# Kernel tuning notes

Hardware: AMD Instinct MI355X
Metric: run time of the kernel (lower is better)

Reference implementation:

```python
import jax, jax.numpy as jnp
import numpy as np

D = 1024   # feature_dim
K = 10     # num_anchors
B = 16384  # batch
H = 8      # num_heads


def setup_inputs() -> dict:
    key = jax.random.key(0)
    ks = jax.random.split(key, 12)
    f32 = jnp.float32

    def w(k, shape, scale=0.02):
        return (jax.random.normal(k, shape, f32) * scale)

    return {
        "features": jax.random.normal(ks[0], (B, D), f32),
        "anchors": w(ks[1], (K, D), 0.1),
        # anchor_refiner: Linear(D, D//2) -> ReLU -> Linear(D//2, D) -> Tanh
        "ar_w1": w(ks[2], (D, D // 2)), "ar_b1": jnp.zeros((D // 2,), f32),
        "ar_w2": w(ks[3], (D // 2, D)), "ar_b2": jnp.zeros((D,), f32),
        # attention projections
        "q_w": w(ks[4], (D, D)), "q_b": jnp.zeros((D,), f32),
        "k_w": w(ks[5], (D, D)), "k_b": jnp.zeros((D,), f32),
        "v_w": w(ks[6], (D, D)), "v_b": jnp.zeros((D,), f32),
        "o_w": w(ks[7], (D, D)), "o_b": jnp.zeros((D,), f32),
        # feature_enhancer: LayerNorm -> Linear(D,2D) -> GELU -> Linear(2D,D)
        "ln_g": jnp.ones((D,), f32), "ln_b": jnp.zeros((D,), f32),
        "ff_w1": w(ks[8], (D, 2 * D)), "ff_b1": jnp.zeros((2 * D,), f32),
        "ff_w2": w(ks[9], (2 * D, D)), "ff_b2": jnp.zeros((D,), f32),
        "div_w": jnp.asarray(0.001, f32),
        "cen_w": jnp.asarray(0.001, f32),
    }


def _l2norm(x, eps=1e-8):
    n = jnp.linalg.norm(x, axis=-1, keepdims=True)
    return x / jnp.maximum(n, eps)


def _layernorm(x, g, b, eps=1e-5):
    mu = jnp.mean(x, axis=-1, keepdims=True)
    var = jnp.mean(jnp.square(x - mu), axis=-1, keepdims=True)
    return (x - mu) * jax.lax.rsqrt(var + eps) * g + b


def reference(features, anchors, ar_w1, ar_b1, ar_w2, ar_b2,
              q_w, q_b, k_w, k_b, v_w, v_b, o_w, o_b,
              ln_g, ln_b, ff_w1, ff_b1, ff_w2, ff_b2, div_w, cen_w):
    b = features.shape[0]
    hd = D // H
    fn = _l2norm(features)                                 # [B, D]

    # anchor refinement
    refin = jnp.tanh(jax.nn.relu(anchors @ ar_w1 + ar_b1) @ ar_w2 + ar_b2)
    an = _l2norm(anchors + 0.1 * refin)                    # [K, D]

    # multi-head cross-attention to anchors
    q = (fn @ q_w + q_b).reshape(b, H, hd)                 # [B, H, hd]
    k = (an @ k_w + k_b).reshape(K, H, hd)                 # [K, H, hd]
    v = (an @ v_w + v_b).reshape(K, H, hd)
    scores = jnp.einsum('bhd,khd->bhk', q, k) / jnp.sqrt(jnp.asarray(hd, fn.dtype))
    aw = jax.nn.softmax(scores, axis=-1)                   # [B, H, K]
    att = jnp.einsum('bhk,khd->bhd', aw, v).reshape(b, D)
    att = att @ o_w + o_b

    # feature enhancer (dropout inactive: eval mode)
    enh = fn + 0.1 * att
    h = jax.nn.gelu(_layernorm(enh, ln_g, ln_b) @ ff_w1 + ff_b1, approximate=False)
    enh = h @ ff_w2 + ff_b2
    final = fn + 0.2 * enh                                 # [B, D]

    # diversity loss: pdist over K=10 anchors (45 pairs)
    diff = an[:, None, :] - an[None, :, :]                 # [K, K, D]
    dmat = jnp.sqrt(jnp.maximum(jnp.sum(diff * diff, -1), 1e-24))
    iu = np.triu_indices(K, 1)
    div_loss = jnp.exp(-jnp.maximum(dmat[iu].mean(), 1e-6))

    # center loss: attention-weighted feature-anchor distances
    avg_att = aw.mean(axis=1)                              # [B, K]
    sq = (jnp.sum(fn * fn, 1, keepdims=True) + jnp.sum(an * an, 1)
          - 2.0 * fn @ an.T)
    fa_dist = jnp.sqrt(jnp.maximum(sq, 1e-12))             # [B, K]
    center_loss = jnp.sum(avg_att * fa_dist, axis=1).mean()

    geo = jnp.abs(div_w) * div_loss + jnp.abs(cen_w) * center_loss
    geo = jnp.clip(geo, 0.0, 0.01)
    return final, geo
```

## Files before the change

### kernel.cpp

```cpp
#include <hip/hip_runtime.h>
#include <hip/hip_bf16.h>
#include <math.h>

typedef __hip_bfloat16 bf16;

#define D_  1024
#define K_  10
#define B_  16384
#define H_  8
#define HD_ 128

struct alignas(16) BF8 { bf16 v[8]; };
struct alignas(8)  BF4 { bf16 v[4]; };

typedef __bf16 bf8v __attribute__((ext_vector_type(8)));
typedef float  f4v  __attribute__((ext_vector_type(4)));

__device__ __forceinline__ float b2f(bf16 x){ return __bfloat162float(x); }
__device__ __forceinline__ bf16  f2b(float x){ return __float2bfloat16(x); }

#define GL2LDS16(g, l) __builtin_amdgcn_global_load_lds( \
    (__attribute__((address_space(1))) void*)(g), \
    (__attribute__((address_space(3))) void*)(l), 16, 0, 0)

__global__ __launch_bounds__(256) void l2norm_k(const float* __restrict__ x,
                                                bf16* __restrict__ fnb) {
  int b = blockIdx.x, t = threadIdx.x;
  float4 v = ((const float4*)(x + (size_t)b * D_))[t];
  float p = v.x*v.x + v.y*v.y + v.z*v.z + v.w*v.w;
  #pragma unroll
  for (int o = 32; o > 0; o >>= 1) p += __shfl_down(p, o);
  __shared__ float wsum[4];
  if ((t & 63) == 0) wsum[t >> 6] = p;
  __syncthreads();
  __shared__ float inv_s;
  if (t == 0) inv_s = 1.f / fmaxf(sqrtf(wsum[0]+wsum[1]+wsum[2]+wsum[3]), 1e-8f);
  __syncthreads();
  float iv = inv_s;
  BF4 o;
  o.v[0] = f2b(v.x*iv); o.v[1] = f2b(v.y*iv);
  o.v[2] = f2b(v.z*iv); o.v[3] = f2b(v.w*iv);
  ((BF4*)(fnb + (size_t)b * D_))[t] = o;
}

__global__ __launch_bounds__(256) void wt3_k(
    const float* __restrict__ qw, const float* __restrict__ w1,
    const float* __restrict__ w2,
    bf16* __restrict__ o_qw, bf16* __restrict__ o_w1, bf16* __restrict__ o_w2) {
  __shared__ float tle[32][33];
  int b = blockIdx.x;
  const float* w; bf16* wt; int R, C, c0, r0;
  if (b < 1024)      { w = qw; wt = o_qw; R = 1024; C = 1024;
                       c0 = (b & 31) * 32;      r0 = (b >> 5) * 32; }
  else if (b < 3072) { int i = b - 1024; w = w1; wt = o_w1; R = 1024; C = 2048;
                       c0 = (i % 64) * 32;      r0 = (i / 64) * 32; }
  else               { int i = b - 3072; w = w2; wt = o_w2; R = 2048; C = 1024;
                       c0 = (i % 32) * 32;      r0 = (i / 32) * 32; }
  int tx = threadIdx.x & 31, ty = threadIdx.x >> 5;
  #pragma unroll
  for (int i = 0; i < 32; i += 8)
    tle[ty + i][tx] = w[(size_t)(r0 + ty + i) * C + c0 + tx];
  __syncthreads();
  #pragma unroll
  for (int i = 0; i < 32; i += 8)
    wt[(size_t)(c0 + ty + i) * R + r0 + tx] = f2b(tle[tx][ty + i]);
}

template<int COLS, int KD, int ACT>
__global__ __launch_bounds__(256) void panelmm_k(
    const float* __restrict__ A, const float* __restrict__ W,
    const float* __restrict__ bias, const float* __restrict__ aux,
    float* __restrict__ out,
    const float* __restrict__ W2, const float* __restrict__ bias2,
    float* __restrict__ out2, int N, int npanel) {
  constexpr int GROUPS = 256 / COLS;
  constexpr int DCH = KD / GROUPS;
  __shared__ float A_s[K_][KD];
  __shared__ float part[K_][COLS][GROUPS];
  const int t = threadIdx.x;
  int blk = blockIdx.x;
  const float* Wm = W; const float* bm = bias; float* om = out;
  if (blk >= npanel) { blk -= npanel; Wm = W2; bm = bias2; om = out2; }
  const int panel = blk;
  for (int i = t; i < K_*KD; i += 256) A_s[0][i] = A[i];
  __syncthreads();
  const int cg = t % COLS, g = t / COLS;
  const int col = panel*COLS + cg;
  float s[K_];
  #pragma unroll
  for (int r = 0; r < K_; ++r) s[r] = 0.f;
  const float* wp = Wm + (size_t)(g*DCH)*N + col;
  for (int d = g*DCH; d < (g+1)*DCH; ++d) {
    float wv = *wp; wp += N;
    #pragma unroll
    for (int r = 0; r < K_; ++r) s[r] = fmaf(A_s[r][d], wv, s[r]);
  }
  #pragma unroll
  for (int r = 0; r < K_; ++r) part[r][cg][g] = s[r];
  __syncthreads();
  for (int o = t; o < K_*COLS; o += 256) {
    int r = o / COLS, c = o % COLS;
    float v = 0.f;
    #pragma unroll
    for (int gg = 0; gg < GROUPS; ++gg) v += part[r][c][gg];
    v += bm[panel*COLS + c];
    if constexpr (ACT == 1) v = fmaxf(v, 0.f);
    if constexpr (ACT == 2) v = aux[(size_t)r*N + panel*COLS + c] + 0.1f*tanhf(v);
    om[(size_t)r*N + panel*COLS + c] = v;
  }
}

__global__ __launch_bounds__(256) void ar3_k(const float* __restrict__ an_un,
    float* __restrict__ an, float* __restrict__ na, float* __restrict__ divloss) {
  __shared__ float a_s[K_][D_];
  __shared__ float nrm[K_];
  __shared__ float dm[45];
  const int t = threadIdx.x;
  for (int i = t; i < K_*D_; i += 256) a_s[0][i] = an_un[i];
  __syncthreads();
  const int wid = t >> 6, lane = t & 63;
  for (int r = wid; r < K_; r += 4) {
    float p = 0.f;
    for (int j = lane; j < D_; j += 64) p += a_s[r][j]*a_s[r][j];
    #pragma unroll
    for (int o = 1; o < 64; o <<= 1) p += __shfl_xor(p, o);
    if (lane == 0) nrm[r] = p;
  }
  __syncthreads();
  for (int i = t; i < K_*D_; i += 256) {
    int r = i >> 10;
    float iv = 1.f / fmaxf(sqrtf(nrm[r]), 1e-8f);
    float v = a_s[0][i] * iv;
    a_s[0][i] = v;
    an[i] = v;
  }
  if (t < K_) {
    float iv = 1.f / fmaxf(sqrtf(nrm[t]), 1e-8f);
    na[t] = nrm[t] * iv * iv;
  }
  __syncthreads();
  const int pr = t >> 2, sub = t & 3;
  if (pr < 45) {
    int i = 0, j = 0, c = pr;
    for (i = 0; i < K_; ++i) { int cnt = K_-1-i; if (c < cnt) { j = i+1+c; break; } c -= cnt; }
    float s = 0.f;
    for (int d = sub*256; d < sub*256 + 256; ++d) {
      float df = a_s[i][d] - a_s[j][d]; s += df*df;
    }
    s += __shfl_xor(s, 1); s += __shfl_xor(s, 2);
    if (sub == 0) dm[pr] = sqrtf(fmaxf(s, 1e-24f));
  }
  __syncthreads();
  if (t == 0) {
    float m = 0.f;
    for (int p = 0; p < 45; ++p) m += dm[p];
    m *= (1.f/45.f);
    *divloss = expf(-fmaxf(m, 1e-6f));
  }
}

template<int TRANSOUT, typename TW>
__device__ __forceinline__ void smallmm_body(
    int blk, const float* __restrict__ A, const TW* __restrict__ W,
    bf16* __restrict__ outb, float scale,
    float (&A_s)[K_][128], float (&part)[K_][64][4]) {
  constexpr int COLS = 64, GROUPS = 4, DCH = 32, NW = 1024;
  const int t = threadIdx.x;
  const int h = blk & 7, panel = blk >> 3;
  for (int i = t; i < K_*128; i += 256) {
    int r = i >> 7, j = i & 127;
    A_s[r][j] = A[r*1024 + h*128 + j];
  }
  __syncthreads();
  const int cg = t % COLS, g = t / COLS;
  const int col = panel*COLS + cg;
  float s[K_];
  #pragma unroll
  for (int r = 0; r < K_; ++r) s[r] = 0.f;
  const TW* wp = W + (size_t)(h*128 + g*DCH)*NW + col;
  for (int d = 0; d < DCH; ++d) {
    float wv;
    if constexpr (sizeof(TW) == 2) wv = b2f(*wp); else wv = *wp;
    wp += NW;
    #pragma unroll
    for (int r = 0; r < K_; ++r) s[r] = fmaf(A_s[r][g*DCH + d], wv, s[r]);
  }
  #pragma unroll
  for (int r = 0; r < K_; ++r) part[r][cg][g] = s[r];
  __syncthreads();
  for (int o = t; o < 16*COLS; o += 256) {
    int r = o / COLS, c = o % COLS;
    float v = 0.f;
    if (r < K_) {
      #pragma unroll
      for (int gg = 0; gg < GROUPS; ++gg) v += part[r][c][gg];
      v *= scale;
    }
    if constexpr (TRANSOUT) outb[(size_t)(panel*COLS + c)*128 + h*16 + r] = f2b(v);
    else                    outb[(size_t)(h*16 + r)*NW + panel*COLS + c] = f2b(v);
  }
}

__global__ __launch_bounds__(256) void prep_k(
    const float* __restrict__ Km, const float* __restrict__ Vm,
    const float* __restrict__ an, const float* __restrict__ na,
    const bf16* __restrict__ wq, const float* __restrict__ ow,
    const float* __restrict__ qb,
    bf16* __restrict__ wt, bf16* __restrict__ vt, float* __restrict__ sb) {
  __shared__ float A_s[K_][128];
  __shared__ float part[K_][64][4];
  const int b = blockIdx.x;
  if (b < 128) {
    smallmm_body<0, bf16>(b, Km, wq, wt, 0.08838834764831845f, A_s, part);
  } else if (b < 256) {
    smallmm_body<1, float>(b - 128, Vm, ow, vt, 1.f, A_s, part);
  } else if (b < 384) {
    int k = b - 256;
    bf16* dst = wt + (size_t)(128 + k) * 1024;
    int i = threadIdx.x * 4;
    BF4 o;
    if (k < K_) {
      float4 a = *(const float4*)(an + (size_t)k*1024 + i);
      o.v[0] = f2b(-2.f*a.x); o.v[1] = f2b(-2.f*a.y);
      o.v[2] = f2b(-2.f*a.z); o.v[3] = f2b(-2.f*a.w);
    } else {
      o.v[0] = o.v[1] = o.v[2] = o.v[3] = f2b(0.f);
    }
    *(BF4*)(dst + i) = o;
  } else {
    int c = threadIdx.x;
    if (c < 128) {
      int h = c >> 4, k = c & 15;
      float s = 0.f;
      if (k < K_) {
        for (int j = 0; j < HD_; ++j)
          s = fmaf(qb[h*HD_ + j], Km[(size_t)k*D_ + h*HD_ + j], s);
      }
      sb[c] = s * 0.08838834764831845f;
    } else {
      int j = c - 128;
      sb[c] = (j < K_) ? (1.f + na[j]) : 0.f;
    }
  }
}

template<int EPI, int KD, typename TO>
__global__ __launch_bounds__(256) void mgemm_k(
    const bf16* __restrict__ A, const bf16* __restrict__ Bt,
    const float* __restrict__ bias, const bf16* __restrict__ aux,
    TO* __restrict__ out, int M, int N, float scale) {
  constexpr int BM = 128, BN = 128, BK = 32;
  constexpr int nt = KD / BK;
  __shared__ bf16 As[2][BM*BK];
  __shared__ bf16 Bs[2][BN*BK];
  const int tid = threadIdx.x;
  const int nMB = M / BM;
  const int nwg = gridDim.x;
  int wg = blockIdx.x;
  wg = (wg & 7) * (nwg >> 3) + (wg >> 3);
  const int bm = (wg % nMB) * BM, bn = (wg / nMB) * BN;

  const int srow = tid >> 2;
  const int ssw  = (((tid & 3) ^ ((tid >> 3) & 3)) * 8);
  const bf16* gA = A  + (size_t)(bm + srow) * KD + ssw;
  const bf16* gB = Bt + (size_t)(bn + srow) * KD + ssw;
  const size_t rstep = (size_t)64 * KD;

  const int w    = tid >> 6;
  const int lane = tid & 63;
  const int wr = (w >> 1) * 64, wc = (w & 1) * 64;
  const int fr = lane & 15, fg = lane >> 4;
  const int key = (fr >> 1) & 3;
  const int co  = (fg ^ key) * 8;

  f4v acc[4][4];
  const f4v zz = {0.f, 0.f, 0.f, 0.f};
  #pragma unroll
  for (int m = 0; m < 4; ++m)
    #pragma unroll
    for (int n = 0; n < 4; ++n) acc[m][n] = zz;

  GL2LDS16(gA,         &As[0][0] + tid*8);
  GL2LDS16(gA + rstep, &As[0][0] + tid*8 + 2048);
  GL2LDS16(gB,         &Bs[0][0] + tid*8);
  GL2LDS16(gB + rstep, &Bs[0][0] + tid*8 + 2048);
  __syncthreads();

  #pragma unroll 2
  for (int t = 0; t < nt; ++t) {
    const int buf = t & 1;
    if (t + 1 < nt) {
      const int ko = (t + 1) * BK;
      GL2LDS16(gA + ko,         &As[buf^1][0] + tid*8);
      GL2LDS16(gA + rstep + ko, &As[buf^1][0] + tid*8 + 2048);
      GL2LDS16(gB + ko,         &Bs[buf^1][0] + tid*8);
      GL2LDS16(gB + rstep + ko, &Bs[buf^1][0] + tid*8 + 2048);
    }
    const bf16* la = &As[buf][0];
    const bf16* lb = &Bs[buf][0];
    bf8v af[4], bq[4];
    #pragma unroll
    for (int m = 0; m < 4; ++m)
      af[m] = *(const bf8v*)(la + (wr + m*16 + fr)*BK + co);
    #pragma unroll
    for (int n = 0; n < 4; ++n)
      bq[n] = *(const bf8v*)(lb + (wc + n*16 + fr)*BK + co);
    __builtin_amdgcn_s_setprio(1);
    #pragma unroll
    for (int m = 0; m < 4; ++m)
      #pragma unroll
      for (int n = 0; n < 4; ++n)
        acc[m][n] = __builtin_amdgcn_mfma_f32_16x16x32_bf16(af[m], bq[n], acc[m][n], 0, 0, 0);
    __builtin_amdgcn_s_setprio(0);
    __syncthreads();
  }

  float bv[4];
  #pragma unroll
  for (int n = 0; n < 4; ++n) bv[n] = bias[bn + wc + n*16 + fr];
  #pragma unroll
  for (int m = 0; m < 4; ++m) {
    #pragma unroll
    for (int r = 0; r < 4; ++r) {
      const int row = bm + wr + m*16 + fg*4 + r;
      #pragma unroll
      for (int n = 0; n < 4; ++n) {
        const int col = bn + wc + n*16 + fr;
        float x = acc[m][n][r] + bv[n];
        if constexpr (EPI == 1) x = b2f(aux[(size_t)row * N + col]) + scale * x;
        if constexpr (EPI == 2) x = 0.5f * x * (1.f + erff(x * 0.70710678118654752f));
        if constexpr (sizeof(TO) == 2) out[(size_t)row * N + col] = f2b(x);
        else                           out[(size_t)row * N + col] = x;
      }
    }
  }
}

template<int EPI, int KD, typename TO>
__global__ __launch_bounds__(512) void mgemm256_k(
    const bf16* __restrict__ A, const bf16* __restrict__ Bt,
    const float* __restrict__ bias, const bf16* __restrict__ aux,
    TO* __restrict__ out, int M, int N, float scale) {
  constexpr int BM = 256, BN = 256, BK = 64;
  constexpr int nt = KD / BK;
  __shared__ bf16 As[2][BM*BK];
  __shared__ bf16 Bs[2][BN*BK];
  const int tid = threadIdx.x;
  const int nMB = M / BM;
  const int nwg = gridDim.x;
  int wg = blockIdx.x;
  wg = (wg & 7) * (nwg >> 3) + (wg >> 3);
  const int bm = (wg % nMB) * BM, bn = (wg / nMB) * BN;

  const int srow = tid >> 3;
  const int scsw = ((tid & 7) ^ (srow & 7)) * 8;
  const bf16* gA = A  + (size_t)(bm + srow) * KD + scsw;
  const bf16* gB = Bt + (size_t)(bn + srow) * KD + scsw;
  const size_t lstep = (size_t)64 * KD;

  const int wid = tid >> 6, lane = tid & 63;
  const int wm = wid >> 2, wn = wid & 3;
  const int fr = lane & 15, fg = lane >> 4;
  const int fsw = fr & 7;
  const int c0 = ((fg     ^ fsw) * 8);
  const int c1 = (((4+fg) ^ fsw) * 8);

  f4v acc[8][4];
  const f4v zz = {0.f, 0.f, 0.f, 0.f};
  #pragma unroll
  for (int m = 0; m < 8; ++m)
    #pragma unroll
    for (int n = 0; n < 4; ++n) acc[m][n] = zz;

  #pragma unroll
  for (int l = 0; l < 4; ++l) {
    GL2LDS16(gA + l*lstep, &As[0][0] + tid*8 + l*4096);
    GL2LDS16(gB + l*lstep, &Bs[0][0] + tid*8 + l*4096);
  }
  __syncthreads();

  #pragma unroll 2
  for (int t = 0; t < nt; ++t) {
    const int buf = t & 1;
    if (t + 1 < nt) {
      const int ko = (t + 1) * BK;
      #pragma unroll
      for (int l = 0; l < 4; ++l) {
        GL2LDS16(gA + l*lstep + ko, &As[buf^1][0] + tid*8 + l*4096);
        GL2LDS16(gB + l*lstep + ko, &Bs[buf^1][0] + tid*8 + l*4096);
      }
    }
    const bf16* la = &As[buf][0];
    const bf16* lb = &Bs[buf][0];
    bf8v bq[8];
    #pragma unroll
    for (int n = 0; n < 4; ++n) {
      const int rb = wn*64 + n*16 + fr;
      bq[n*2]   = *(const bf8v*)(lb + rb*64 + c0);
      bq[n*2+1] = *(const bf8v*)(lb + rb*64 + c1);
    }
    __builtin_amdgcn_s_setprio(1);
    #pragma unroll
    for (int m = 0; m < 8; ++m) {
      const int ra = wm*128 + m*16 + fr;
      bf8v a0 = *(const bf8v*)(la + ra*64 + c0);
      bf8v a1 = *(const bf8v*)(la + ra*64 + c1);
      #pragma unroll
      for (int n = 0; n < 4; ++n) {
        acc[m][n] = __builtin_amdgcn_mfma_f32_16x16x32_bf16(a0, bq[n*2],   acc[m][n], 0, 0, 0);
        acc[m][n] = __builtin_amdgcn_mfma_f32_16x16x32_bf16(a1, bq[n*2+1], acc[m][n], 0, 0, 0);
      }
    }
    __builtin_amdgcn_s_setprio(0);
    __syncthreads();
  }

  float bv[4];
  #pragma unroll
  for (int n = 0; n < 4; ++n) bv[n] = bias[bn + wn*64 + n*16 + fr];
  #pragma unroll
  for (int m = 0; m < 8; ++m) {
    #pragma unroll
    for (int r = 0; r < 4; ++r) {
      const int row = bm + wm*128 + m*16 + fg*4 + r;
      #pragma unroll
      for (int n = 0; n < 4; ++n) {
        const int col = bn + wn*64 + n*16 + fr;
        float x = acc[m][n][r] + bv[n];
        if constexpr (EPI == 1) x = b2f(aux[(size_t)row * N + col]) + scale * x;
        if constexpr (EPI == 2) x = 0.5f * x * (1.f + erff(x * 0.70710678118654752f));
        if constexpr (sizeof(TO) == 2) out[(size_t)row * N + col] = f2b(x);
        else                           out[(size_t)row * N + col] = x;
      }
    }
  }
}

__global__ __launch_bounds__(256) void attn2_k(
    const float* __restrict__ S, bf16* __restrict__ awp,
    float* __restrict__ cen_acc) {
  __shared__ float cred[4];
  const int t = threadIdx.x;
  const int wid = t >> 6, lane = t & 63;
  const int sub = lane & 7, head = lane >> 3;
  const int k0 = sub*2, k1 = k0 + 1;
  float c_acc = 0.f;
  const int row0 = blockIdx.x * 32 + wid * 8;

  for (int i = 0; i < 8; ++i) {
    const int row = row0 + i;
    const float* Sr = S + (size_t)row * 256;
    float2 sv = *(const float2*)(Sr + head*16 + k0);
    float v0 = (k0 < K_) ? sv.x : -1e30f;
    float v1 = (k1 < K_) ? sv.y : -1e30f;
    float m = fmaxf(v0, v1);
    m = fmaxf(m, __shfl_xor(m,1)); m = fmaxf(m, __shfl_xor(m,2)); m = fmaxf(m, __shfl_xor(m,4));
    float e0 = (k0 < K_) ? __expf(v0 - m) : 0.f;
    float e1 = (k1 < K_) ? __expf(v1 - m) : 0.f;
    float es = e0 + e1;
    es += __shfl_xor(es,1); es += __shfl_xor(es,2); es += __shfl_xor(es,4);
    float inv = 1.f / es;
    float a0 = e0 * inv, a1 = e1 * inv;
    bf16 b0 = f2b(a0), b1 = f2b(a1);
    unsigned int pk = (unsigned int)(*(unsigned short*)&b0)
                    | ((unsigned int)(*(unsigned short*)&b1) << 16);
    *(unsigned int*)(awp + (size_t)row*128 + head*16 + k0) = pk;
    float g0 = a0, g1 = a1;
    g0 += __shfl_xor(g0,8); g0 += __shfl_xor(g0,16); g0 += __shfl_xor(g0,32);
    g1 += __shfl_xor(g1,8); g1 += __shfl_xor(g1,16); g1 += __shfl_xor(g1,32);
    if (sub < 5) {
      float d20 = Sr[128 + k0];
      float d21 = Sr[128 + k1];
      c_acc = fmaf(g0, sqrtf(fmaxf(d20, 1e-12f)), c_acc);
      c_acc = fmaf(g1, sqrtf(fmaxf(d21, 1e-12f)), c_acc);
    }
  }
  #pragma unroll
  for (int o = 1; o < 64; o <<= 1) c_acc += __shfl_xor(c_acc, o);
  if (lane == 0) cred[wid] = c_acc;
  __syncthreads();
  if (t == 0) {
    float s = (cred[0]+cred[1]+cred[2]+cred[3]) * (1.f/64.f/(float)B_);
    atomicAdd(cen_acc, s);
  }
}

__global__ __launch_bounds__(256) void ln_k(const bf16* __restrict__ x,
    const float* __restrict__ g, const float* __restrict__ bta,
    bf16* __restrict__ out) {
  int b = blockIdx.x, t = threadIdx.x;
  BF4 ld = ((const BF4*)(x + (size_t)b * D_))[t];
  float v[4];
  #pragma unroll
  for (int j = 0; j < 4; ++j) v[j] = b2f(ld.v[j]);
  float s = v[0]+v[1]+v[2]+v[3];
  #pragma unroll
  for (int o = 32; o > 0; o >>= 1) s += __shfl_down(s, o);
  __shared__ float w1[4], w2[4];
  if ((t & 63) == 0) w1[t >> 6] = s;
  __syncthreads();
  __shared__ float mu_s, rs_s;
  if (t == 0) mu_s = (w1[0]+w1[1]+w1[2]+w1[3]) * (1.f/D_);
  __syncthreads();
  float mu = mu_s;
  float qv = 0.f;
  #pragma unroll
  for (int j = 0; j < 4; ++j) { float d = v[j]-mu; qv += d*d; }
  #pragma unroll
  for (int o = 32; o > 0; o >>= 1) qv += __shfl_down(qv, o);
  if ((t & 63) == 0) w2[t >> 6] = qv;
  __syncthreads();
  if (t == 0) rs_s = rsqrtf((w2[0]+w2[1]+w2[2]+w2[3]) * (1.f/D_) + 1e-5f);
  __syncthreads();
  float rs = rs_s;
  BF4 o;
  #pragma unroll
  for (int j = 0; j < 4; ++j) {
    int col = t*4 + j;
    o.v[j] = f2b((v[j]-mu)*rs*g[col] + bta[col]);
  }
  ((BF4*)(out + (size_t)b * D_))[t] = o;
}

__global__ void geo_k(const float* __restrict__ divl, const float* __restrict__ cen,
                      const float* __restrict__ div_w, const float* __restrict__ cen_w,
                      float* __restrict__ out) {
  float g = fabsf(*div_w) * (*divl) + fabsf(*cen_w) * (*cen);
  out[0] = fminf(fmaxf(g, 0.f), 0.01f);
}

extern "C" void kernel_launch(void* const* d_in, const int* in_sizes, int n_in,
                              void* d_out, int out_size, void* d_ws, size_t ws_size,
                              hipStream_t stream) {
  const float* features = (const float*)d_in[0];
  const float* anchors  = (const float*)d_in[1];
  const float* ar_w1 = (const float*)d_in[2];
  const float* ar_b1 = (const float*)d_in[3];
  const float* ar_w2 = (const float*)d_in[4];
  const float* ar_b2 = (const float*)d_in[5];
  const float* q_w = (const float*)d_in[6];
  const float* q_b = (const float*)d_in[7];
  const float* k_w = (const float*)d_in[8];
  const float* k_b = (const float*)d_in[9];
  const float* v_w = (const float*)d_in[10];
  const float* v_b = (const float*)d_in[11];
  const float* o_w = (const float*)d_in[12];
  const float* o_b = (const float*)d_in[13];
  const float* ln_g = (const float*)d_in[14];
  const float* ln_b = (const float*)d_in[15];
  const float* ff_w1 = (const float*)d_in[16];
  const float* ff_b1 = (const float*)d_in[17];
  const float* ff_w2 = (const float*)d_in[18];
  const float* ff_b2 = (const float*)d_in[19];
  const float* div_w = (const float*)d_in[20];
  const float* cen_w = (const float*)d_in[21];
  float* out = (float*)d_out;

  char* w = (char*)d_ws;
  bf16* ws_fnb = (bf16*)w;  w += (size_t)B_ * D_ * 2;
  bf16* ws_enh = (bf16*)w;  w += (size_t)B_ * D_ * 2;
  bf16* ws_ln  = (bf16*)w;  w += (size_t)B_ * D_ * 2;
  bf16* ws_h   = (bf16*)w;  w += (size_t)B_ * 2048 * 2;
  float* ws_S  = (float*)w; w += (size_t)B_ * 256 * 4;
  bf16* ws_awp = (bf16*)w;  w += (size_t)B_ * 128 * 2;
  bf16* ws_wq  = (bf16*)w;  w += (size_t)D_ * D_ * 2;
  bf16* ws_w1t = (bf16*)w;  w += (size_t)D_ * 2048 * 2;
  bf16* ws_w2t = (bf16*)w;  w += (size_t)2048 * D_ * 2;
  bf16* ws_wt  = (bf16*)w;  w += (size_t)256 * D_ * 2;
  bf16* ws_vt  = (bf16*)w;  w += (size_t)D_ * 128 * 2;
  float* ws_har = (float*)w;  w += (size_t)K_ * (D_/2) * 4;
  float* ws_anu = (float*)w;  w += (size_t)K_ * D_ * 4;
  float* ws_an  = (float*)w;  w += (size_t)K_ * D_ * 4;
  float* ws_k   = (float*)w;  w += (size_t)K_ * D_ * 4;
  float* ws_v   = (float*)w;  w += (size_t)K_ * D_ * 4;
  float* ws_na  = (float*)w;  w += 256;
  float* ws_div = (float*)w;  w += 256;
  float* ws_cen = (float*)w;  w += 256;
  float* ws_sb  = (float*)w;  w += 512;
  if ((size_t)(w - (char*)d_ws) > ws_size) return;

  hipMemsetAsync(ws_cen, 0, 4, stream);

  wt3_k<<<5120, 256, 0, stream>>>(q_w, ff_w1, ff_w2, ws_wq, ws_w1t, ws_w2t);

  l2norm_k<<<B_, 256, 0, stream>>>(features, ws_fnb);

  panelmm_k<32, 1024, 1><<<16, 256, 0, stream>>>(
      anchors, ar_w1, ar_b1, nullptr, ws_har,
      nullptr, nullptr, nullptr, D_/2, 16);
  panelmm_k<64, 512, 2><<<16, 256, 0, stream>>>(
      ws_har, ar_w2, ar_b2, anchors, ws_anu,
      nullptr, nullptr, nullptr, D_, 16);
  ar3_k<<<1, 256, 0, stream>>>(ws_anu, ws_an, ws_na, ws_div);
  panelmm_k<64, 1024, 0><<<32, 256, 0, stream>>>(
      ws_an, k_w, k_b, nullptr, ws_k,
      v_w, v_b, ws_v, D_, 16);

  prep_k<<<385, 256, 0, stream>>>(ws_k, ws_v, ws_an, ws_na,
                                  ws_wq, o_w, q_b, ws_wt, ws_vt, ws_sb);

  mgemm_k<0, 1024, float><<<dim3((B_/128)*(256/128)), 256, 0, stream>>>(
      ws_fnb, ws_wt, ws_sb, nullptr, ws_S, B_, 256, 0.f);

  attn2_k<<<B_/32, 256, 0, stream>>>(ws_S, ws_awp, ws_cen);

  mgemm_k<1, 128, bf16><<<dim3((B_/128)*(D_/128)), 256, 0, stream>>>(
      ws_awp, ws_vt, o_b, ws_fnb, ws_enh, B_, D_, 0.1f);

  ln_k<<<B_, 256, 0, stream>>>(ws_enh, ln_g, ln_b, ws_ln);

  mgemm256_k<2, 1024, bf16><<<dim3((B_/256)*(2048/256)), 512, 0, stream>>>(
      ws_ln, ws_w1t, ff_b1, nullptr, ws_h, B_, 2048, 0.f);

  mgemm256_k<1, 2048, float><<<dim3((B_/256)*(D_/256)), 512, 0, stream>>>(
      ws_h, ws_w2t, ff_b2, ws_fnb, out, B_, D_, 0.2f);

  geo_k<<<1, 1, 0, stream>>>(ws_div, ws_cen, div_w, cen_w, out + (size_t)B_ * D_);
}
```

Measured before the change: 399.7 us.

## Triple-buffer 256x256 GEMM with BK=32 and split A/B staging phases

Restructures the 256x256 bf16 MFMA GEMM main loop. It uses a three-stage LDS ring with a 32-wide K step in place of double buffering with a 64-wide step, and prefetches two tiles ahead. Each iteration is split into two half-compute phases, with the A and B global-to-LDS loads issued between them. Explicit vmcnt waits and raw s_barrier replace __syncthreads so loads overlap more with MFMA work. In exchange there are more barriers per K element and a new swizzle pattern, which could add sync overhead or bank conflicts.

```diff
diff --git a/kernel.cpp b/kernel.cpp
--- a/kernel.cpp
+++ b/kernel.cpp
@@ -341,10 +341,10 @@
     const bf16* __restrict__ A, const bf16* __restrict__ Bt,
     const float* __restrict__ bias, const bf16* __restrict__ aux,
     TO* __restrict__ out, int M, int N, float scale) {
-  constexpr int BM = 256, BN = 256, BK = 64;
+  constexpr int BM = 256, BN = 256, BK = 32;
   constexpr int nt = KD / BK;
-  __shared__ bf16 As[2][BM*BK];
-  __shared__ bf16 Bs[2][BN*BK];
+  __shared__ bf16 As[3][BM*BK];
+  __shared__ bf16 Bs[3][BN*BK];
   const int tid = threadIdx.x;
   const int nMB = M / BM;
   const int nwg = gridDim.x;
@@ -352,18 +352,25 @@
   wg = (wg & 7) * (nwg >> 3) + (wg >> 3);
   const int bm = (wg % nMB) * BM, bn = (wg / nMB) * BN;
 
-  const int srow = tid >> 3;
-  const int scsw = ((tid & 7) ^ (srow & 7)) * 8;
-  const bf16* gA = A  + (size_t)(bm + srow) * KD + scsw;
-  const bf16* gB = Bt + (size_t)(bn + srow) * KD + scsw;
-  const size_t lstep = (size_t)64 * KD;
+  const int srow = tid >> 2;
+  const int ssw  = (((tid & 3) ^ ((tid >> 3) & 3)) * 8);
+  const bf16* gA = A  + (size_t)(bm + srow) * KD + ssw;
+  const bf16* gB = Bt + (size_t)(bn + srow) * KD + ssw;
+  const size_t rstep = (size_t)128 * KD;
+
+#define STG_A(sl, kt) do { \
+    GL2LDS16(gA + (size_t)(kt)*BK,         &As[sl][0] + tid*8); \
+    GL2LDS16(gA + rstep + (size_t)(kt)*BK, &As[sl][0] + tid*8 + 4096); \
+  } while(0)
+#define STG_B(sl, kt) do { \
+    GL2LDS16(gB + (size_t)(kt)*BK,         &Bs[sl][0] + tid*8); \
+    GL2LDS16(gB + rstep + (size_t)(kt)*BK, &Bs[sl][0] + tid*8 + 4096); \
+  } while(0)
 
   const int wid = tid >> 6, lane = tid & 63;
   const int wm = wid >> 2, wn = wid & 3;
   const int fr = lane & 15, fg = lane >> 4;
-  const int fsw = fr & 7;
-  const int c0 = ((fg     ^ fsw) * 8);
-  const int c1 = (((4+fg) ^ fsw) * 8);
+  const int co = ((fg ^ ((fr >> 1) & 3)) * 8);
 
   f4v acc[8][4];
   const f4v zz = {0.f, 0.f, 0.f, 0.f};
@@ -372,47 +379,50 @@
     #pragma unroll
     for (int n = 0; n < 4; ++n) acc[m][n] = zz;
 
-  #pragma unroll
-  for (int l = 0; l < 4; ++l) {
-    GL2LDS16(gA + l*lstep, &As[0][0] + tid*8 + l*4096);
-    GL2LDS16(gB + l*lstep, &Bs[0][0] + tid*8 + l*4096);
-  }
-  __syncthreads();
-
-  #pragma unroll 2
+  STG_A(0, 0); STG_B(0, 0);
+  STG_A(1, 1); STG_B(1, 1);
+  asm volatile("s_waitcnt vmcnt(4)" ::: "memory");
+  __builtin_amdgcn_s_barrier();
+
+  int s0 = 0, s1 = 1, s2 = 2;
   for (int t = 0; t < nt; ++t) {
-    const int buf = t & 1;
-    if (t + 1 < nt) {
-      const int ko = (t + 1) * BK;
-      #pragma unroll
-      for (int l = 0; l < 4; ++l) {
-        GL2LDS16(gA + l*lstep + ko, &As[buf^1][0] + tid*8 + l*4096);
-        GL2LDS16(gB + l*lstep + ko, &Bs[buf^1][0] + tid*8 + l*4096);
-      }
-    }
-    const bf16* la = &As[buf][0];
-    const bf16* lb = &Bs[buf][0];
-    bf8v bq[8];
-    #pragma unroll
-    for (int n = 0; n < 4; ++n) {
-      const int rb = wn*64 + n*16 + fr;
-      bq[n*2]   = *(const bf8v*)(lb + rb*64 + c0);
-      bq[n*2+1] = *(const bf8v*)(lb + rb*64 + c1);
-    }
+    const bf16* la = &As[s0][0];
+    const bf16* lb = &Bs[s0][0];
+    const int arow = wm*128 + fr;
+    const int brow = wn*64 + fr;
+    bf8v af[8], bq0, bq1;
+    if (t + 2 < nt) STG_A(s2, t + 2);
+    #pragma unroll
+    for (int m = 0; m < 8; ++m)
+      af[m] = *(const bf8v*)(la + (arow + m*16)*BK + co);
+    bq0 = *(const bf8v*)(lb + (brow     )*BK + co);
+    bq1 = *(const bf8v*)(lb + (brow + 16)*BK + co);
+    __builtin_amdgcn_sched_barrier(0);
+    __builtin_amdgcn_s_barrier();
     __builtin_amdgcn_s_setprio(1);
     #pragma unroll
     for (int m = 0; m < 8; ++m) {
-      const int ra = wm*128 + m*16 + fr;
-      bf8v a0 = *(const bf8v*)(la + ra*64 + c0);
-      bf8v a1 = *(const bf8v*)(la + ra*64 + c1);
-      #pragma unroll
-      for (int n = 0; n < 4; ++n) {
-        acc[m][n] = __builtin_amdgcn_mfma_f32_16x16x32_bf16(a0, bq[n*2],   acc[m][n], 0, 0, 0);
-        acc[m][n] = __builtin_amdgcn_mfma_f32_16x16x32_bf16(a1, bq[n*2+1], acc[m][n], 0, 0, 0);
-      }
+      acc[m][0] = __builtin_amdgcn_mfma_f32_16x16x32_bf16(af[m], bq0, acc[m][0], 0, 0, 0);
+      acc[m][1] = __builtin_amdgcn_mfma_f32_16x16x32_bf16(af[m], bq1, acc[m][1], 0, 0, 0);
     }
     __builtin_amdgcn_s_setprio(0);
-    __syncthreads();
+    __builtin_amdgcn_s_barrier();
+    if (t + 2 < nt) STG_B(s2, t + 2);
+    bf8v bq2 = *(const bf8v*)(lb + (brow + 32)*BK + co);
+    bf8v bq3 = *(const bf8v*)(lb + (brow + 48)*BK + co);
+    __builtin_amdgcn_sched_barrier(0);
+    if (t + 2 < nt) asm volatile("s_waitcnt vmcnt(4)" ::: "memory");
+    else            asm volatile("s_waitcnt vmcnt(0)" ::: "memory");
+    __builtin_amdgcn_s_barrier();
+    __builtin_amdgcn_s_setprio(1);
+    #pragma unroll
+    for (int m = 0; m < 8; ++m) {
+      acc[m][2] = __builtin_amdgcn_mfma_f32_16x16x32_bf16(af[m], bq2, acc[m][2], 0, 0, 0);
+      acc[m][3] = __builtin_amdgcn_mfma_f32_16x16x32_bf16(af[m], bq3, acc[m][3], 0, 0, 0);
+    }
+    __builtin_amdgcn_s_setprio(0);
+    __builtin_amdgcn_s_barrier();
+    int tmp = s0; s0 = s1; s1 = s2; s2 = tmp;
   }
 
   float bv[4];
@@ -434,6 +444,8 @@
       }
     }
   }
+#undef STG_A
+#undef STG_B
 }
 
 __global__ __launch_bounds__(256) void attn2_k(
```

Measured after the change: 474.5 us. +18.7%, slower.

## Fuse score GEMM with softmax/center loss and o-proj GEMM with LayerNorm

Applied to the files above, without the earlier changes.

The score GEMM now does softmax, attention-weight writing and the center-loss reduction in its epilogue, using 64-row tiles that span all 256 score columns. This removes the fp32 S buffer and the separate attention kernel. The o-projection GEMM now covers full 1024-column rows per block, so it can apply the residual and the LayerNorm statistics in its epilogue. That removes the enh buffer round trip and the standalone LayerNorm kernel. In exchange, LayerNorm variance is computed as E[x²]−mu², which is less numerically stable, and the larger per-block tiles (a 64 KB B buffer in enhln, a 32-tile accumulator) may cut occupancy.

```diff
diff --git a/kernel.cpp b/kernel.cpp
--- a/kernel.cpp
+++ b/kernel.cpp
@@ -244,46 +244,45 @@
   }
 }
 
-template<int EPI, int KD, typename TO>
-__global__ __launch_bounds__(256) void mgemm_k(
+__global__ __launch_bounds__(256) void sattn_k(
     const bf16* __restrict__ A, const bf16* __restrict__ Bt,
-    const float* __restrict__ bias, const bf16* __restrict__ aux,
-    TO* __restrict__ out, int M, int N, float scale) {
-  constexpr int BM = 128, BN = 128, BK = 32;
-  constexpr int nt = KD / BK;
-  __shared__ bf16 As[2][BM*BK];
-  __shared__ bf16 Bs[2][BN*BK];
+    const float* __restrict__ sb, bf16* __restrict__ awp,
+    float* __restrict__ cen_acc) {
+  constexpr int BK = 32, KD = 1024, nt = KD / BK;
+  __shared__ bf16 As[2][64*BK];
+  __shared__ bf16 Bs[2][256*BK];
+  __shared__ float d2buf[64][16];
+  __shared__ float cred[2];
   const int tid = threadIdx.x;
-  const int nMB = M / BM;
   const int nwg = gridDim.x;
   int wg = blockIdx.x;
   wg = (wg & 7) * (nwg >> 3) + (wg >> 3);
-  const int bm = (wg % nMB) * BM, bn = (wg / nMB) * BN;
-
-  const int srow = tid >> 2;
-  const int ssw  = (((tid & 3) ^ ((tid >> 3) & 3)) * 8);
-  const bf16* gA = A  + (size_t)(bm + srow) * KD + ssw;
-  const bf16* gB = Bt + (size_t)(bn + srow) * KD + ssw;
-  const size_t rstep = (size_t)64 * KD;
-
-  const int w    = tid >> 6;
-  const int lane = tid & 63;
-  const int wr = (w >> 1) * 64, wc = (w & 1) * 64;
+  const int bm = wg * 64;
+
+  const int arow_s = tid >> 2;
+  const int assw = (((tid & 3) ^ ((arow_s >> 1) & 3)) * 8);
+  const bf16* gA = A + (size_t)(bm + arow_s) * KD + assw;
+
+  const int wid = tid >> 6, lane = tid & 63;
+  const int wm = wid >> 1, wn = wid & 1;
   const int fr = lane & 15, fg = lane >> 4;
-  const int key = (fr >> 1) & 3;
-  const int co  = (fg ^ key) * 8;
-
-  f4v acc[4][4];
+  const int co = ((fg ^ ((fr >> 1) & 3)) * 8);
+
+  f4v acc[2][8];
   const f4v zz = {0.f, 0.f, 0.f, 0.f};
   #pragma unroll
-  for (int m = 0; m < 4; ++m)
-    #pragma unroll
-    for (int n = 0; n < 4; ++n) acc[m][n] = zz;
-
-  GL2LDS16(gA,         &As[0][0] + tid*8);
-  GL2LDS16(gA + rstep, &As[0][0] + tid*8 + 2048);
-  GL2LDS16(gB,         &Bs[0][0] + tid*8);
-  GL2LDS16(gB + rstep, &Bs[0][0] + tid*8 + 2048);
+  for (int m = 0; m < 2; ++m)
+    #pragma unroll
+    for (int n = 0; n < 8; ++n) acc[m][n] = zz;
+
+  GL2LDS16(gA, &As[0][0] + tid*8);
+  #pragma unroll
+  for (int l = 0; l < 4; ++l) {
+    const int c = l*256 + tid;
+    const int brow = c >> 2;
+    const int bsw = (((c & 3) ^ ((brow >> 1) & 3)) * 8);
+    GL2LDS16(Bt + (size_t)brow * KD + bsw, &Bs[0][0] + tid*8 + l*2048);
+  }
   __syncthreads();
 
   #pragma unroll 2
@@ -291,46 +290,221 @@
     const int buf = t & 1;
     if (t + 1 < nt) {
       const int ko = (t + 1) * BK;
-      GL2LDS16(gA + ko,         &As[buf^1][0] + tid*8);
-      GL2LDS16(gA + rstep + ko, &As[buf^1][0] + tid*8 + 2048);
-      GL2LDS16(gB + ko,         &Bs[buf^1][0] + tid*8);
-      GL2LDS16(gB + rstep + ko, &Bs[buf^1][0] + tid*8 + 2048);
+      GL2LDS16(gA + ko, &As[buf^1][0] + tid*8);
+      #pragma unroll
+      for (int l = 0; l < 4; ++l) {
+        const int c = l*256 + tid;
+        const int brow = c >> 2;
+        const int bsw = (((c & 3) ^ ((brow >> 1) & 3)) * 8);
+        GL2LDS16(Bt + (size_t)brow * KD + bsw + ko, &Bs[buf^1][0] + tid*8 + l*2048);
+      }
     }
     const bf16* la = &As[buf][0];
     const bf16* lb = &Bs[buf][0];
-    bf8v af[4], bq[4];
-    #pragma unroll
-    for (int m = 0; m < 4; ++m)
-      af[m] = *(const bf8v*)(la + (wr + m*16 + fr)*BK + co);
-    #pragma unroll
-    for (int n = 0; n < 4; ++n)
-      bq[n] = *(const bf8v*)(lb + (wc + n*16 + fr)*BK + co);
+    bf8v af[2], bq[8];
+    #pragma unroll
+    for (int m = 0; m < 2; ++m)
+      af[m] = *(const bf8v*)(la + (wm*32 + m*16 + fr)*BK + co);
+    #pragma unroll
+    for (int n = 0; n < 8; ++n)
+      bq[n] = *(const bf8v*)(lb + (wn*128 + n*16 + fr)*BK + co);
     __builtin_amdgcn_s_setprio(1);
     #pragma unroll
-    for (int m = 0; m < 4; ++m)
-      #pragma unroll
-      for (int n = 0; n < 4; ++n)
+    for (int m = 0; m < 2; ++m)
+      #pragma unroll
+      for (int n = 0; n < 8; ++n)
         acc[m][n] = __builtin_amdgcn_mfma_f32_16x16x32_bf16(af[m], bq[n], acc[m][n], 0, 0, 0);
     __builtin_amdgcn_s_setprio(0);
     __syncthreads();
   }
 
-  float bv[4];
-  #pragma unroll
-  for (int n = 0; n < 4; ++n) bv[n] = bias[bn + wc + n*16 + fr];
+  float gaw[2][4];
+  #pragma unroll
+  for (int m = 0; m < 2; ++m)
+    #pragma unroll
+    for (int r = 0; r < 4; ++r) gaw[m][r] = 0.f;
+
+  if (wn == 0) {
+    #pragma unroll
+    for (int n = 0; n < 8; ++n) {
+      const float sbv = sb[n*16 + fr];
+      #pragma unroll
+      for (int m = 0; m < 2; ++m) {
+        #pragma unroll
+        for (int r = 0; r < 4; ++r) {
+          float v = acc[m][n][r] + sbv;
+          float vm = (fr < K_) ? v : -1e30f;
+          vm = fmaxf(vm, __shfl_xor(vm, 1)); vm = fmaxf(vm, __shfl_xor(vm, 2));
+          vm = fmaxf(vm, __shfl_xor(vm, 4)); vm = fmaxf(vm, __shfl_xor(vm, 8));
+          float e = (fr < K_) ? __expf(v - vm) : 0.f;
+          float es = e;
+          es += __shfl_xor(es, 1); es += __shfl_xor(es, 2);
+          es += __shfl_xor(es, 4); es += __shfl_xor(es, 8);
+          float aw = e / es;
+          const int row = bm + wm*32 + m*16 + fg*4 + r;
+          awp[(size_t)row * 128 + n*16 + fr] = f2b(aw);
+          gaw[m][r] += aw;
+        }
+      }
+    }
+  } else {
+    const float sbd = sb[128 + fr];
+    #pragma unroll
+    for (int m = 0; m < 2; ++m)
+      #pragma unroll
+      for (int r = 0; r < 4; ++r)
+        d2buf[wm*32 + m*16 + fg*4 + r][fr] = acc[m][0][r] + sbd;
+  }
+  __syncthreads();
+  float c_acc = 0.f;
+  if (wn == 0) {
+    #pragma unroll
+    for (int m = 0; m < 2; ++m) {
+      #pragma unroll
+      for (int r = 0; r < 4; ++r) {
+        float d2 = d2buf[wm*32 + m*16 + fg*4 + r][fr];
+        float contrib = (fr < K_) ? gaw[m][r] * sqrtf(fmaxf(d2, 1e-12f)) : 0.f;
+        contrib += __shfl_xor(contrib, 1); contrib += __shfl_xor(contrib, 2);
+        contrib += __shfl_xor(contrib, 4); contrib += __shfl_xor(contrib, 8);
+        if (fr == 0) c_acc += contrib;
+      }
+    }
+    #pragma unroll
+    for (int o = 1; o < 64; o <<= 1) c_acc += __shfl_xor(c_acc, o);
+    if (lane == 0) cred[wm] = c_acc;
+  }
+  __syncthreads();
+  if (tid == 0)
+    atomicAdd(cen_acc, (cred[0] + cred[1]) * (0.125f / (float)B_));
+}
+
+__global__ __launch_bounds__(512) void enhln_k(
+    const bf16* __restrict__ A, const bf16* __restrict__ Bt,
+    const float* __restrict__ ob, const bf16* __restrict__ aux,
+    const float* __restrict__ ln_g, const float* __restrict__ ln_b,
+    bf16* __restrict__ out) {
+  constexpr int BK = 32, KD = 128, nt = KD / BK;
+  __shared__ bf16 As[2][64*BK];
+  __shared__ bf16 Bs[2][1024*BK];
+  __shared__ float stat[64][8][2];
+  const int tid = threadIdx.x;
+  const int nwg = gridDim.x;
+  int wg = blockIdx.x;
+  wg = (wg & 7) * (nwg >> 3) + (wg >> 3);
+  const int bm = wg * 64;
+
+  const int arow_s = tid >> 2;
+  const int assw = (((tid & 3) ^ ((arow_s >> 1) & 3)) * 8);
+  const bf16* gA = A + (size_t)(bm + arow_s) * KD + assw;
+
+  const int wid = tid >> 6, lane = tid & 63;
+  const int wn = wid;
+  const int fr = lane & 15, fg = lane >> 4;
+  const int co = ((fg ^ ((fr >> 1) & 3)) * 8);
+
+  f4v acc[4][8];
+  const f4v zz = {0.f, 0.f, 0.f, 0.f};
+  #pragma unroll
+  for (int m = 0; m < 4; ++m)
+    #pragma unroll
+    for (int n = 0; n < 8; ++n) acc[m][n] = zz;
+
+  if (tid < 256) GL2LDS16(gA, &As[0][0] + tid*8);
+  #pragma unroll
+  for (int l = 0; l < 8; ++l) {
+    const int c = l*512 + tid;
+    const int brow = c >> 2;
+    const int bsw = (((c & 3) ^ ((brow >> 1) & 3)) * 8);
+    GL2LDS16(Bt + (size_t)brow * KD + bsw, &Bs[0][0] + tid*8 + l*4096);
+  }
+  __syncthreads();
+
+  #pragma unroll
+  for (int t = 0; t < nt; ++t) {
+    const int buf = t & 1;
+    if (t + 1 < nt) {
+      const int ko = (t + 1) * BK;
+      if (tid < 256) GL2LDS16(gA + ko, &As[buf^1][0] + tid*8);
+      #pragma unroll
+      for (int l = 0; l < 8; ++l) {
+        const int c = l*512 + tid;
+        const int brow = c >> 2;
+        const int bsw = (((c & 3) ^ ((brow >> 1) & 3)) * 8);
+        GL2LDS16(Bt + (size_t)brow * KD + bsw + ko, &Bs[buf^1][0] + tid*8 + l*4096);
+      }
+    }
+    const bf16* la = &As[buf][0];
+    const bf16* lb = &Bs[buf][0];
+    bf8v af[4], bq[8];
+    #pragma unroll
+    for (int m = 0; m < 4; ++m)
+      af[m] = *(const bf8v*)(la + (m*16 + fr)*BK + co);
+    #pragma unroll
+    for (int n = 0; n < 8; ++n)
+      bq[n] = *(const bf8v*)(lb + (wn*128 + n*16 + fr)*BK + co);
+    __builtin_amdgcn_s_setprio(1);
+    #pragma unroll
+    for (int m = 0; m < 4; ++m)
+      #pragma unroll
+      for (int n = 0; n < 8; ++n)
+        acc[m][n] = __builtin_amdgcn_mfma_f32_16x16x32_bf16(af[m], bq[n], acc[m][n], 0, 0, 0);
+    __builtin_amdgcn_s_setprio(0);
+    __syncthreads();
+  }
+
+  #pragma unroll
+  for (int n = 0; n < 8; ++n) {
+    const int col = wn*128 + n*16 + fr;
+    const float obv = ob[col];
+    #pragma unroll
+    for (int m = 0; m < 4; ++m) {
+      #pragma unroll
+      for (int r = 0; r < 4; ++r) {
+        const int row = bm + m*16 + fg*4 + r;
+        acc[m][n][r] = b2f(aux[(size_t)row * D_ + col]) + 0.1f*(acc[m][n][r] + obv);
+      }
+    }
+  }
   #pragma unroll
   for (int m = 0; m < 4; ++m) {
     #pragma unroll
     for (int r = 0; r < 4; ++r) {
-      const int row = bm + wr + m*16 + fg*4 + r;
-      #pragma unroll
-      for (int n = 0; n < 4; ++n) {
-        const int col = bn + wc + n*16 + fr;
-        float x = acc[m][n][r] + bv[n];
-        if constexpr (EPI == 1) x = b2f(aux[(size_t)row * N + col]) + scale * x;
-        if constexpr (EPI == 2) x = 0.5f * x * (1.f + erff(x * 0.70710678118654752f));
-        if constexpr (sizeof(TO) == 2) out[(size_t)row * N + col] = f2b(x);
-        else                           out[(size_t)row * N + col] = x;
+      float s1 = 0.f, s2 = 0.f;
+      #pragma unroll
+      for (int n = 0; n < 8; ++n) { float x = acc[m][n][r]; s1 += x; s2 += x*x; }
+      s1 += __shfl_xor(s1, 1); s1 += __shfl_xor(s1, 2);
+      s1 += __shfl_xor(s1, 4); s1 += __shfl_xor(s1, 8);
+      s2 += __shfl_xor(s2, 1); s2 += __shfl_xor(s2, 2);
+      s2 += __shfl_xor(s2, 4); s2 += __shfl_xor(s2, 8);
+      if (fr == 0) {
+        stat[m*16 + fg*4 + r][wn][0] = s1;
+        stat[m*16 + fg*4 + r][wn][1] = s2;
+      }
+    }
+  }
+  __syncthreads();
+  float gv[8], bvv[8];
+  #pragma unroll
+  for (int n = 0; n < 8; ++n) {
+    const int col = wn*128 + n*16 + fr;
+    gv[n] = ln_g[col]; bvv[n] = ln_b[col];
+  }
+  #pragma unroll
+  for (int m = 0; m < 4; ++m) {
+    #pragma unroll
+    for (int r = 0; r < 4; ++r) {
+      const int lr = m*16 + fg*4 + r;
+      float S1 = 0.f, S2 = 0.f;
+      #pragma unroll
+      for (int w = 0; w < 8; ++w) { S1 += stat[lr][w][0]; S2 += stat[lr][w][1]; }
+      const float mu = S1 * (1.f/1024.f);
+      const float var = S2 * (1.f/1024.f) - mu*mu;
+      const float rstd = rsqrtf(var + 1e-5f);
+      const int row = bm + lr;
+      #pragma unroll
+      for (int n = 0; n < 8; ++n) {
+        const int col = wn*128 + n*16 + fr;
+        out[(size_t)row * D_ + col] = f2b((acc[m][n][r] - mu)*rstd*gv[n] + bvv[n]);
       }
     }
   }
@@ -434,92 +608,6 @@
       }
     }
   }
-}
-
-__global__ __launch_bounds__(256) void attn2_k(
-    const float* __restrict__ S, bf16* __restrict__ awp,
-    float* __restrict__ cen_acc) {
-  __shared__ float cred[4];
-  const int t = threadIdx.x;
-  const int wid = t >> 6, lane = t & 63;
-  const int sub = lane & 7, head = lane >> 3;
-  const int k0 = sub*2, k1 = k0 + 1;
-  float c_acc = 0.f;
-  const int row0 = blockIdx.x * 32 + wid * 8;
-
-  for (int i = 0; i < 8; ++i) {
-    const int row = row0 + i;
-    const float* Sr = S + (size_t)row * 256;
-    float2 sv = *(const float2*)(Sr + head*16 + k0);
-    float v0 = (k0 < K_) ? sv.x : -1e30f;
-    float v1 = (k1 < K_) ? sv.y : -1e30f;
-    float m = fmaxf(v0, v1);
-    m = fmaxf(m, __shfl_xor(m,1)); m = fmaxf(m, __shfl_xor(m,2)); m = fmaxf(m, __shfl_xor(m,4));
-    float e0 = (k0 < K_) ? __expf(v0 - m) : 0.f;
-    float e1 = (k1 < K_) ? __expf(v1 - m) : 0.f;
-    float es = e0 + e1;
-    es += __shfl_xor(es,1); es += __shfl_xor(es,2); es += __shfl_xor(es,4);
-    float inv = 1.f / es;
-    float a0 = e0 * inv, a1 = e1 * inv;
-    bf16 b0 = f2b(a0), b1 = f2b(a1);
-    unsigned int pk = (unsigned int)(*(unsigned short*)&b0)
-                    | ((unsigned int)(*(unsigned short*)&b1) << 16);
-    *(unsigned int*)(awp + (size_t)row*128 + head*16 + k0) = pk;
-    float g0 = a0, g1 = a1;
-    g0 += __shfl_xor(g0,8); g0 += __shfl_xor(g0,16); g0 += __shfl_xor(g0,32);
-    g1 += __shfl_xor(g1,8); g1 += __shfl_xor(g1,16); g1 += __shfl_xor(g1,32);
-    if (sub < 5) {
-      float d20 = Sr[128 + k0];
-      float d21 = Sr[128 + k1];
-      c_acc = fmaf(g0, sqrtf(fmaxf(d20, 1e-12f)), c_acc);
-      c_acc = fmaf(g1, sqrtf(fmaxf(d21, 1e-12f)), c_acc);
-    }
-  }
-  #pragma unroll
-  for (int o = 1; o < 64; o <<= 1) c_acc += __shfl_xor(c_acc, o);
-  if (lane == 0) cred[wid] = c_acc;
-  __syncthreads();
-  if (t == 0) {
-    float s = (cred[0]+cred[1]+cred[2]+cred[3]) * (1.f/64.f/(float)B_);
-    atomicAdd(cen_acc, s);
-  }
-}
-
-__global__ __launch_bounds__(256) void ln_k(const bf16* __restrict__ x,
-    const float* __restrict__ g, const float* __restrict__ bta,
-    bf16* __restrict__ out) {
-  int b = blockIdx.x, t = threadIdx.x;
-  BF4 ld = ((const BF4*)(x + (size_t)b * D_))[t];
-  float v[4];
-  #pragma unroll
-  for (int j = 0; j < 4; ++j) v[j] = b2f(ld.v[j]);
-  float s = v[0]+v[1]+v[2]+v[3];
-  #pragma unroll
-  for (int o = 32; o > 0; o >>= 1) s += __shfl_down(s, o);
-  __shared__ float w1[4], w2[4];
-  if ((t & 63) == 0) w1[t >> 6] = s;
-  __syncthreads();
-  __shared__ float mu_s, rs_s;
-  if (t == 0) mu_s = (w1[0]+w1[1]+w1[2]+w1[3]) * (1.f/D_);
-  __syncthreads();
-  float mu = mu_s;
-  float qv = 0.f;
-  #pragma unroll
-  for (int j = 0; j < 4; ++j) { float d = v[j]-mu; qv += d*d; }
-  #pragma unroll
-  for (int o = 32; o > 0; o >>= 1) qv += __shfl_down(qv, o);
-  if ((t & 63) == 0) w2[t >> 6] = qv;
-  __syncthreads();
-  if (t == 0) rs_s = rsqrtf((w2[0]+w2[1]+w2[2]+w2[3]) * (1.f/D_) + 1e-5f);
-  __syncthreads();
-  float rs = rs_s;
-  BF4 o;
-  #pragma unroll
-  for (int j = 0; j < 4; ++j) {
-    int col = t*4 + j;
-    o.v[j] = f2b((v[j]-mu)*rs*g[col] + bta[col]);
-  }
-  ((BF4*)(out + (size_t)b * D_))[t] = o;
 }
 
 __global__ void geo_k(const float* __restrict__ divl, const float* __restrict__ cen,
@@ -558,10 +646,8 @@
 
   char* w = (char*)d_ws;
   bf16* ws_fnb = (bf16*)w;  w += (size_t)B_ * D_ * 2;
-  bf16* ws_enh = (bf16*)w;  w += (size_t)B_ * D_ * 2;
   bf16* ws_ln  = (bf16*)w;  w += (size_t)B_ * D_ * 2;
   bf16* ws_h   = (bf16*)w;  w += (size_t)B_ * 2048 * 2;
-  float* ws_S  = (float*)w; w += (size_t)B_ * 256 * 4;
   bf16* ws_awp = (bf16*)w;  w += (size_t)B_ * 128 * 2;
   bf16* ws_wq  = (bf16*)w;  w += (size_t)D_ * D_ * 2;
   bf16* ws_w1t = (bf16*)w;  w += (size_t)D_ * 2048 * 2;
@@ -599,15 +685,10 @@
   prep_k<<<385, 256, 0, stream>>>(ws_k, ws_v, ws_an, ws_na,
                                   ws_wq, o_w, q_b, ws_wt, ws_vt, ws_sb);
 
-  mgemm_k<0, 1024, float><<<dim3((B_/128)*(256/128)), 256, 0, stream>>>(
-      ws_fnb, ws_wt, ws_sb, nullptr, ws_S, B_, 256, 0.f);
-
-  attn2_k<<<B_/32, 256, 0, stream>>>(ws_S, ws_awp, ws_cen);
-
-  mgemm_k<1, 128, bf16><<<dim3((B_/128)*(D_/128)), 256, 0, stream>>>(
-      ws_awp, ws_vt, o_b, ws_fnb, ws_enh, B_, D_, 0.1f);
-
-  ln_k<<<B_, 256, 0, stream>>>(ws_enh, ln_g, ln_b, ws_ln);
+  sattn_k<<<B_/64, 256, 0, stream>>>(ws_fnb, ws_wt, ws_sb, ws_awp, ws_cen);
+
+  enhln_k<<<B_/64, 512, 0, stream>>>(ws_awp, ws_vt, o_b, ws_fnb,
+                                     ln_g, ln_b, ws_ln);
 
   mgemm256_k<2, 1024, bf16><<<dim3((B_/256)*(2048/256)), 512, 0, stream>>>(
       ws_ln, ws_w1t, ff_b1, nullptr, ws_h, B_, 2048, 0.f);
```

Result: slower. 411.5 us (+2.9%).
